# Kernel tuning notes

Measured on AMD Instinct MI355X. Metric: run time of the kernel, lower is better.

The kernel has to match this reference:

```python
import jax, jax.numpy as jnp
import numpy as np

B, T, C, H = 4, 4096, 1024, 64  # batch, seq, n_embd, head_size

def setup_inputs() -> dict:
    key = jax.random.key(0)
    kx, kq, kk, kv = jax.random.split(key, 4)
    x = jax.random.normal(kx, (B, T, C), dtype=jnp.float32)
    s = 1.0 / np.sqrt(C)
    Wq = jax.random.normal(kq, (C, H), dtype=jnp.float32) * s
    Wk = jax.random.normal(kk, (C, H), dtype=jnp.float32) * s
    Wv = jax.random.normal(kv, (C, H), dtype=jnp.float32) * s
    return {"x": x, "Wq": Wq, "Wk": Wk, "Wv": Wv}

def reference(x, Wq, Wk, Wv):
    B_, T_, C_ = x.shape
    q = x @ Wq  # [B,T,H]
    k = x @ Wk
    v = x @ Wv
    # NOTE: original scales by C**-0.5 (n_embd), not head_size**-0.5
    scale = jnp.asarray(C_, x.dtype) ** -0.5
    wei = jnp.einsum('bth,bsh->bts', q, k) * scale  # [B,T,T]
    causal = jnp.tril(jnp.ones((T_, T_), dtype=bool))
    wei = jnp.where(causal, wei, -jnp.inf)
    wei = jax.nn.softmax(wei, axis=-1)
    out = jnp.einsum('bts,bsh->bth', wei, v)  # [B,T,H]
    return out
```

## Files before the change

### kernel.cpp

```cpp
#include <hip/hip_runtime.h>
#include <hip/hip_bf16.h>
#include <math.h>

#define BB 4
#define TT 4096
#define CC 1024
#define HH 64

typedef __attribute__((ext_vector_type(8))) short short8;
typedef __attribute__((ext_vector_type(8))) unsigned short ushort8;
typedef __attribute__((ext_vector_type(4))) float f32x4;
typedef __attribute__((ext_vector_type(2))) unsigned int uint2v;
typedef __attribute__((ext_vector_type(4))) unsigned int uint4v;

__device__ inline unsigned short f2bf(float f) {
    unsigned int u = __builtin_bit_cast(unsigned int, f);
    unsigned int r = u + 0x7fffu + ((u >> 16) & 1u);
    return (unsigned short)(r >> 16);
}

__device__ inline unsigned int cvtpk(float lo, float hi) {
    unsigned int r;
    asm("v_cvt_pk_bf16_f32 %0, %1, %2" : "=v"(r) : "v"(lo), "v"(hi));
    return r;
}

__device__ inline int soff_strip(int qs) {
    if (qs < 128) return (qs - 64) * 2;
    if (qs < 192) return 128 + (qs - 128) * 3;
    return 320 + (qs - 192) * 4;
}

__global__ __launch_bounds__(256) void wtrans_kernel(
    const float* __restrict__ Wq,
    const float* __restrict__ Wk,
    const float* __restrict__ Wv,
    unsigned short* __restrict__ Wf)
{
    const int t = blockIdx.x * 256 + threadIdx.x;
    const int lane = t & 63;
    const int ntl  = (t >> 6) % 12;
    const int kt   = t / 768;
    const int quad = lane >> 4, n = lane & 15;
    const int m    = ntl >> 2;
    const int col  = (ntl & 3) * 16 + n;
    const float* src = (m == 0) ? Wq : (m == 1) ? Wk : Wv;
    ushort8 u;
#pragma unroll
    for (int j = 0; j < 8; ++j)
        u[j] = f2bf(src[(kt * 32 + quad * 8 + j) * 64 + col]);
    *(ushort8*)(Wf + (size_t)t * 8) = u;
}

__global__ __launch_bounds__(256, 4) void qkv_gemm(
    const float* __restrict__ x,
    const unsigned short* __restrict__ Wf,
    unsigned short* __restrict__ Qb,
    unsigned short* __restrict__ Kf,
    unsigned short* __restrict__ Vf)
{
    __shared__ __align__(16) unsigned char smem[25088];
    f32x4 (*red)[12][64] = (f32x4 (*)[12][64])smem;
    float (*Tl)[200]     = (float (*)[200])(smem + 12288);

    const int tid  = threadIdx.x;
    const int lane = tid & 63;
    const int wave = tid >> 6;
    const int n    = lane & 15;
    const int quad = lane >> 4;

    const int row0g = blockIdx.x * 16;
    const int b     = row0g >> 12;
    const int trow  = row0g & (TT - 1);
    const int st    = trow >> 6;
    const int mtb   = (trow >> 4) & 3;
    const int kkv   = (trow >> 5) & 1;
    const int vhalf = (trow >> 4) & 1;

    const float* xp0 = x + (size_t)(row0g + n) * CC + wave * 256 + quad * 8;

    f32x4 acc[12];
#pragma unroll
    for (int i = 0; i < 12; ++i) acc[i] = (f32x4){0.f, 0.f, 0.f, 0.f};

    float4 Pa[3][2];
#pragma unroll
    for (int s = 0; s < 3; ++s) {
        Pa[s][0] = *(const float4*)(xp0 + s * 32);
        Pa[s][1] = *(const float4*)(xp0 + s * 32 + 4);
    }

#pragma unroll
    for (int kt = 0; kt < 8; ++kt) {
        const int sl = kt % 3;

        uint4v u0;
        u0[0] = cvtpk(Pa[sl][0].x, Pa[sl][0].y);
        u0[1] = cvtpk(Pa[sl][0].z, Pa[sl][0].w);
        u0[2] = cvtpk(Pa[sl][1].x, Pa[sl][1].y);
        u0[3] = cvtpk(Pa[sl][1].z, Pa[sl][1].w);
        const short8 a0 = __builtin_bit_cast(short8, u0);

        if (kt + 3 < 8) {
            Pa[sl][0] = *(const float4*)(xp0 + (kt + 3) * 32);
            Pa[sl][1] = *(const float4*)(xp0 + (kt + 3) * 32 + 4);
        }

        const unsigned short* wp = Wf + ((size_t)((wave * 8 + kt) * 12) * 64 + lane) * 8;
#pragma unroll
        for (int ntl = 0; ntl < 12; ++ntl) {
            const short8 bw = *(const short8*)(wp + (size_t)ntl * 64 * 8);
            acc[ntl] = __builtin_amdgcn_mfma_f32_16x16x32_bf16(a0, bw, acc[ntl], 0, 0, 0);
        }
    }

    if (wave >= 2) {
#pragma unroll
        for (int ntl = 0; ntl < 12; ++ntl)
            red[wave - 2][ntl][lane] = acc[ntl];
    }
    __syncthreads();
    if (wave < 2) {
#pragma unroll
        for (int ntl = 0; ntl < 12; ++ntl)
            acc[ntl] += red[wave][ntl][lane];
    }
    __syncthreads();
    if (wave == 1) {
#pragma unroll
        for (int ntl = 0; ntl < 12; ++ntl)
            red[0][ntl][lane] = acc[ntl];
    }
    __syncthreads();
    if (wave == 0) {
#pragma unroll
        for (int ntl = 0; ntl < 12; ++ntl) {
            const f32x4 s = acc[ntl] + red[0][ntl][lane];
            const int col = (ntl >> 2) * 64 + (ntl & 3) * 16 + n;
#pragma unroll
            for (int r = 0; r < 4; ++r)
                Tl[quad * 4 + r][col] = s[r];
        }
    }
    __syncthreads();

    {
        const int row = tid & 15;
        const int c0  = (tid >> 4) * 4;
        unsigned int w0 = cvtpk(Tl[row][c0]     * 0.03125f, Tl[row][c0 + 1] * 0.03125f);
        unsigned int w1 = cvtpk(Tl[row][c0 + 2] * 0.03125f, Tl[row][c0 + 3] * 0.03125f);
        uint2v w; w[0] = w0; w[1] = w1;
        *(uint2v*)(Qb + (size_t)(row0g + row) * HH + c0) = w;
    }
    if (wave < 2) {
        const int kk = wave;
        ushort8 u;
#pragma unroll
        for (int j = 0; j < 8; ++j)
            u[j] = f2bf(Tl[n][64 + kk * 32 + quad * 8 + j]);
        const size_t r = (size_t)(((b * 64 + st) * 4 + mtb) * 2 + kk) * 64 + lane;
        *(ushort8*)(Kf + r * 8) = u;
    } else {
        const int hh = quad >> 1;
        const int ht = (wave - 2) * 2 + hh;
        const int qq = vhalf * 2 + (quad & 1);
        ushort8 u;
#pragma unroll
        for (int j = 0; j < 8; ++j)
            u[j] = f2bf(Tl[(quad & 1) * 8 + j][128 + ht * 16 + n]);
        const size_t r = (size_t)(((b * 64 + st) * 4 + ht) * 2 + kkv) * 64 + qq * 16 + n;
        *(ushort8*)(Vf + r * 8) = u;
    }
}

__global__ __launch_bounds__(256) void attn_kernel(
    const unsigned short* __restrict__ Qb,
    const unsigned short* __restrict__ Kf,
    const unsigned short* __restrict__ Vf,
    float* __restrict__ out,
    float* __restrict__ scr)
{
    __shared__ unsigned short Ps[4][2][16][72];

    const int tid  = threadIdx.x;
    const int lane = tid & 63;
    const int wave = tid >> 6;
    const int n    = lane & 15;
    const int quad = lane >> 4;

    const int wid = blockIdx.x * 4 + wave;
    const int b   = wid / 640;
    const int u   = wid - b * 640;

    int qs, ci;
    if (u < 64)        { qs = u;                  ci = 0; }
    else if (u < 192)  { const int v = u - 64;  qs = 64  + (v >> 1); ci = v & 1; }
    else if (u < 384)  { const int v = u - 192; const int d = v / 3;
                         qs = 128 + d;            ci = v - 3 * d; }
    else               { const int v = u - 384; qs = 192 + (v >> 2); ci = v & 3; }

    const int stmax = qs >> 2;
    const int st0   = ci << 4;
    const int stEnd = min(stmax, st0 + 15);
    const int nc    = (stmax + 16) >> 4;
    const int qrow  = qs * 16 + n;

    const unsigned short* qp = Qb + ((size_t)b * TT + qrow) * HH;
    const short8 bQ0 = *(const short8*)(qp + quad * 8);
    const short8 bQ1 = *(const short8*)(qp + 32 + quad * 8);

    const unsigned short* KfB = Kf + (size_t)b * 262144;
    const unsigned short* VfB = Vf + (size_t)b * 262144;

    f32x4 O[4];
#pragma unroll
    for (int ht = 0; ht < 4; ++ht) O[ht] = (f32x4){0.f, 0.f, 0.f, 0.f};
    float l = 0.f;

    short8 kA[4], kB[4];
#pragma unroll
    for (int mt = 0; mt < 4; ++mt) {
        const unsigned short* kp = KfB + (size_t)((st0 * 4 + mt) * 2) * 512 + lane * 8;
        kA[mt] = *(const short8*)(kp);
        kB[mt] = *(const short8*)(kp + 512);
    }

    for (int st = st0; st <= stEnd; ++st) {
        f32x4 S[4];
#pragma unroll
        for (int mt = 0; mt < 4; ++mt) {
            f32x4 acc = (f32x4){0.f, 0.f, 0.f, 0.f};
            acc = __builtin_amdgcn_mfma_f32_16x16x32_bf16(kA[mt], bQ0, acc, 0, 0, 0);
            acc = __builtin_amdgcn_mfma_f32_16x16x32_bf16(kB[mt], bQ1, acc, 0, 0, 0);
            S[mt] = acc;
        }

        short8 vA[4], vB[4];
#pragma unroll
        for (int ht = 0; ht < 4; ++ht) {
            const unsigned short* vp = VfB + (size_t)((st * 4 + ht) * 2) * 512 + lane * 8;
            vA[ht] = *(const short8*)(vp);
            vB[ht] = *(const short8*)(vp + 512);
        }
        if (st < stEnd) {
#pragma unroll
            for (int mt = 0; mt < 4; ++mt) {
                const unsigned short* kp = KfB + (size_t)(((st + 1) * 4 + mt) * 2) * 512 + lane * 8;
                kA[mt] = *(const short8*)(kp);
                kB[mt] = *(const short8*)(kp + 512);
            }
        }

        if (st == stmax) {
#pragma unroll
            for (int mt = 0; mt < 4; ++mt) {
                const int sg = st * 64 + mt * 16 + quad * 4;
#pragma unroll
                for (int r = 0; r < 4; ++r)
                    if (sg + r > qrow) S[mt][r] = -INFINITY;
            }
        }

#pragma unroll
        for (int mt = 0; mt < 4; ++mt)
#pragma unroll
            for (int r = 0; r < 4; ++r) {
                const float p = __expf(fminf(S[mt][r], 30.f));
                S[mt][r] = p;
                l += p;
            }

        const int pp = st & 1;
#pragma unroll
        for (int mt = 0; mt < 4; ++mt) {
            uint2v w;
            w[0] = (unsigned int)f2bf(S[mt][0]) | ((unsigned int)f2bf(S[mt][1]) << 16);
            w[1] = (unsigned int)f2bf(S[mt][2]) | ((unsigned int)f2bf(S[mt][3]) << 16);
            *(uint2v*)&Ps[wave][pp][n][mt * 16 + quad * 4] = w;
        }
        asm volatile("s_waitcnt lgkmcnt(0)" ::: "memory");
        const short8 bP0 = *(const short8*)&Ps[wave][pp][n][quad * 8];
        const short8 bP1 = *(const short8*)&Ps[wave][pp][n][32 + quad * 8];

#pragma unroll
        for (int ht = 0; ht < 4; ++ht) {
            O[ht] = __builtin_amdgcn_mfma_f32_16x16x32_bf16(vA[ht], bP0, O[ht], 0, 0, 0);
            O[ht] = __builtin_amdgcn_mfma_f32_16x16x32_bf16(vB[ht], bP1, O[ht], 0, 0, 0);
        }
    }

    l += __shfl_xor(l, 16);
    l += __shfl_xor(l, 32);

    if (nc == 1) {
        const float inv = 1.0f / l;
        float* op = out + ((size_t)b * TT + qrow) * HH;
#pragma unroll
        for (int ht = 0; ht < 4; ++ht) {
            float4 o4;
            o4.x = O[ht][0] * inv;
            o4.y = O[ht][1] * inv;
            o4.z = O[ht][2] * inv;
            o4.w = O[ht][3] * inv;
            *(float4*)(op + ht * 16 + quad * 4) = o4;
        }
    } else {
        float* sb = scr + (size_t)(b * 576 + soff_strip(qs) + ci) * 1040;
        float* rp = sb + n * 64;
#pragma unroll
        for (int ht = 0; ht < 4; ++ht)
            *(f32x4*)(rp + ht * 16 + quad * 4) = O[ht];
        if (quad == 0) sb[1024 + n] = l;
    }
}

__global__ __launch_bounds__(64) void combine_kernel(
    const float* __restrict__ scr,
    float* __restrict__ out)
{
    const int b  = blockIdx.x / 192;
    const int qs = 64 + blockIdx.x % 192;
    const int nc = ((qs >> 2) + 16) >> 4;
    const int base = b * 576 + soff_strip(qs);

    const int t    = threadIdx.x;
    const int row  = t >> 2;
    const int col0 = (t & 3) * 16;

    f32x4 s0 = (f32x4){0.f,0.f,0.f,0.f}, s1 = s0, s2 = s0, s3 = s0;
    float lsum = 0.f;
    for (int ci = 0; ci < nc; ++ci) {
        const float* sb = scr + (size_t)(base + ci) * 1040;
        lsum += sb[1024 + row];
        const float* p = sb + row * 64 + col0;
        s0 += *(const f32x4*)(p);
        s1 += *(const f32x4*)(p + 4);
        s2 += *(const f32x4*)(p + 8);
        s3 += *(const f32x4*)(p + 12);
    }
    const float inv = 1.0f / lsum;
    float* op = out + ((size_t)b * TT + qs * 16 + row) * HH + col0;
    *(f32x4*)(op)      = s0 * inv;
    *(f32x4*)(op + 4)  = s1 * inv;
    *(f32x4*)(op + 8)  = s2 * inv;
    *(f32x4*)(op + 12) = s3 * inv;
}

extern "C" void kernel_launch(void* const* d_in, const int* in_sizes, int n_in,
                              void* d_out, int out_size, void* d_ws, size_t ws_size,
                              hipStream_t stream)
{
    const float* x  = (const float*)d_in[0];
    const float* Wq = (const float*)d_in[1];
    const float* Wk = (const float*)d_in[2];
    const float* Wv = (const float*)d_in[3];

    unsigned short* Qb = (unsigned short*)d_ws;
    unsigned short* Wf = Qb + (size_t)BB * TT * HH;
    unsigned short* Kf = Wf + (size_t)192 * 1024;
    unsigned short* Vf = Kf + (size_t)BB * 262144;
    float*          scr = (float*)(Vf + (size_t)BB * 262144);
    float* out = (float*)d_out;

    wtrans_kernel<<<96, 256, 0, stream>>>(Wq, Wk, Wv, Wf);
    qkv_gemm<<<BB * TT / 16, 256, 0, stream>>>(x, Wf, Qb, Kf, Vf);
    attn_kernel<<<640, 256, 0, stream>>>(Qb, Kf, Vf, out, scr);
    combine_kernel<<<768, 64, 0, stream>>>(scr, out);
}
```

Before: 153.4 us.

## Restructure QKV GEMM into 64-row tiles with double-buffered LDS staging

The QKV projection kernel now handles 64 rows per block with 512 threads instead of 16 rows with 256. It stages x and weight tiles into LDS through asynchronous global_load_lds, double-buffered across 16 K-steps, and uses an XOR swizzle on the x tile. Each wave owns one 16-row m-tile and half of the 12 output n-tiles, so the cross-wave split-K reduction goes away. Each weight tile is now reused across four m-tiles rather than being reloaded from global memory per 16-row block. The cost is 80 KB of LDS per block, which limits occupancy, and 256 blocks may underfill the GPU.

```diff
diff --git a/kernel.cpp b/kernel.cpp
--- a/kernel.cpp
+++ b/kernel.cpp
@@ -23,6 +23,13 @@
     unsigned int r;
     asm("v_cvt_pk_bf16_f32 %0, %1, %2" : "=v"(r) : "v"(lo), "v"(hi));
     return r;
+}
+
+__device__ inline void gll16(const void* g, void* l) {
+    __builtin_amdgcn_global_load_lds(
+        (const __attribute__((address_space(1))) unsigned int*)g,
+        (__attribute__((address_space(3))) unsigned int*)l,
+        16, 0, 0);
 }
 
 __device__ inline int soff_strip(int qs) {
@@ -52,123 +59,123 @@
     *(ushort8*)(Wf + (size_t)t * 8) = u;
 }
 
-__global__ __launch_bounds__(256, 4) void qkv_gemm(
+__global__ __launch_bounds__(512, 2) void qkv_gemm(
     const float* __restrict__ x,
     const unsigned short* __restrict__ Wf,
     unsigned short* __restrict__ Qb,
     unsigned short* __restrict__ Kf,
     unsigned short* __restrict__ Vf)
 {
-    __shared__ __align__(16) unsigned char smem[25088];
-    f32x4 (*red)[12][64] = (f32x4 (*)[12][64])smem;
-    float (*Tl)[200]     = (float (*)[200])(smem + 12288);
+    __shared__ __align__(16) unsigned char smem[81920];
+    float (*Tl)[200] = (float (*)[200])smem;
 
     const int tid  = threadIdx.x;
     const int lane = tid & 63;
     const int wave = tid >> 6;
     const int n    = lane & 15;
     const int quad = lane >> 4;
-
-    const int row0g = blockIdx.x * 16;
+    const int mt   = wave & 3;
+    const int ch   = wave >> 2;
+
+    const int row0g = blockIdx.x * 64;
     const int b     = row0g >> 12;
-    const int trow  = row0g & (TT - 1);
-    const int st    = trow >> 6;
-    const int mtb   = (trow >> 4) & 3;
-    const int kkv   = (trow >> 5) & 1;
-    const int vhalf = (trow >> 4) & 1;
-
-    const float* xp0 = x + (size_t)(row0g + n) * CC + wave * 256 + quad * 8;
-
-    f32x4 acc[12];
-#pragma unroll
-    for (int i = 0; i < 12; ++i) acc[i] = (f32x4){0.f, 0.f, 0.f, 0.f};
-
-    float4 Pa[3][2];
-#pragma unroll
-    for (int s = 0; s < 3; ++s) {
-        Pa[s][0] = *(const float4*)(xp0 + s * 32);
-        Pa[s][1] = *(const float4*)(xp0 + s * 32 + 4);
-    }
-
-#pragma unroll
-    for (int kt = 0; kt < 8; ++kt) {
-        const int sl = kt % 3;
-
-        uint4v u0;
-        u0[0] = cvtpk(Pa[sl][0].x, Pa[sl][0].y);
-        u0[1] = cvtpk(Pa[sl][0].z, Pa[sl][0].w);
-        u0[2] = cvtpk(Pa[sl][1].x, Pa[sl][1].y);
-        u0[3] = cvtpk(Pa[sl][1].z, Pa[sl][1].w);
-        const short8 a0 = __builtin_bit_cast(short8, u0);
-
-        if (kt + 3 < 8) {
-            Pa[sl][0] = *(const float4*)(xp0 + (kt + 3) * 32);
-            Pa[sl][1] = *(const float4*)(xp0 + (kt + 3) * 32 + 4);
-        }
-
-        const unsigned short* wp = Wf + ((size_t)((wave * 8 + kt) * 12) * 64 + lane) * 8;
-#pragma unroll
-        for (int ntl = 0; ntl < 12; ++ntl) {
-            const short8 bw = *(const short8*)(wp + (size_t)ntl * 64 * 8);
-            acc[ntl] = __builtin_amdgcn_mfma_f32_16x16x32_bf16(a0, bw, acc[ntl], 0, 0, 0);
-        }
-    }
-
-    if (wave >= 2) {
-#pragma unroll
-        for (int ntl = 0; ntl < 12; ++ntl)
-            red[wave - 2][ntl][lane] = acc[ntl];
-    }
+    const int st    = (row0g & (TT - 1)) >> 6;
+
+    const char* xg = (const char*)(x + (size_t)row0g * CC);
+    const char* wg = (const char*)Wf;
+
+    f32x4 acc[6];
+#pragma unroll
+    for (int i = 0; i < 6; ++i) acc[i] = (f32x4){0.f, 0.f, 0.f, 0.f};
+
+    auto stage = [&](int bb, int s) {
+        unsigned char* base = smem + bb * 40960;
+#pragma unroll
+        for (int i = 0; i < 2; ++i) {
+            const int rr = (i * 8 + wave) * 4 + (lane >> 4);
+            const int cb = ((lane & 15) * 16) ^ ((rr & 7) << 4);
+            gll16(xg + (size_t)rr * 4096 + s * 256 + cb,
+                  base + (i * 8 + wave) * 1024);
+        }
+#pragma unroll
+        for (int i = 0; i < 3; ++i) {
+            const int off = (i * 8 + wave) * 1024;
+            gll16(wg + (size_t)s * 24576 + off + lane * 16,
+                  base + 16384 + off);
+        }
+    };
+
+    auto compute = [&](int bb) {
+        const unsigned char* xb = smem + bb * 40960;
+        const unsigned char* wb = xb + 16384;
+        const int row = mt * 16 + n;
+        const int swz = (n & 7) << 4;
+#pragma unroll
+        for (int ktl = 0; ktl < 2; ++ktl) {
+            const int c0 = (ktl * 128 + quad * 32) ^ swz;
+            const int c1 = (ktl * 128 + quad * 32 + 16) ^ swz;
+            const float4 f0 = *(const float4*)(xb + row * 256 + c0);
+            const float4 f1 = *(const float4*)(xb + row * 256 + c1);
+            uint4v u;
+            u[0] = cvtpk(f0.x, f0.y);
+            u[1] = cvtpk(f0.z, f0.w);
+            u[2] = cvtpk(f1.x, f1.y);
+            u[3] = cvtpk(f1.z, f1.w);
+            const short8 a0 = __builtin_bit_cast(short8, u);
+#pragma unroll
+            for (int t = 0; t < 6; ++t) {
+                const int g = ch * 6 + t;
+                const short8 bwv = *(const short8*)(wb + (ktl * 12 + g) * 1024 + lane * 16);
+                acc[t] = __builtin_amdgcn_mfma_f32_16x16x32_bf16(a0, bwv, acc[t], 0, 0, 0);
+            }
+        }
+    };
+
+    stage(0, 0);
     __syncthreads();
-    if (wave < 2) {
-#pragma unroll
-        for (int ntl = 0; ntl < 12; ++ntl)
-            acc[ntl] += red[wave][ntl][lane];
+#pragma unroll 2
+    for (int s = 0; s < 16; ++s) {
+        if (s + 1 < 16) stage((s + 1) & 1, s + 1);
+        compute(s & 1);
+        __syncthreads();
+    }
+
+#pragma unroll
+    for (int t = 0; t < 6; ++t) {
+        const int g   = ch * 6 + t;
+        const int col = (g >> 2) * 64 + (g & 3) * 16 + n;
+#pragma unroll
+        for (int r = 0; r < 4; ++r)
+            Tl[mt * 16 + quad * 4 + r][col] = acc[t][r];
     }
     __syncthreads();
-    if (wave == 1) {
-#pragma unroll
-        for (int ntl = 0; ntl < 12; ++ntl)
-            red[0][ntl][lane] = acc[ntl];
-    }
-    __syncthreads();
-    if (wave == 0) {
-#pragma unroll
-        for (int ntl = 0; ntl < 12; ++ntl) {
-            const f32x4 s = acc[ntl] + red[0][ntl][lane];
-            const int col = (ntl >> 2) * 64 + (ntl & 3) * 16 + n;
-#pragma unroll
-            for (int r = 0; r < 4; ++r)
-                Tl[quad * 4 + r][col] = s[r];
-        }
-    }
-    __syncthreads();
 
     {
-        const int row = tid & 15;
-        const int c0  = (tid >> 4) * 4;
-        unsigned int w0 = cvtpk(Tl[row][c0]     * 0.03125f, Tl[row][c0 + 1] * 0.03125f);
-        unsigned int w1 = cvtpk(Tl[row][c0 + 2] * 0.03125f, Tl[row][c0 + 3] * 0.03125f);
-        uint2v w; w[0] = w0; w[1] = w1;
-        *(uint2v*)(Qb + (size_t)(row0g + row) * HH + c0) = w;
-    }
-    if (wave < 2) {
-        const int kk = wave;
+        const int row = tid & 63;
+        const int c0  = (tid >> 6) * 8;
+        uint4v w4;
+        w4[0] = cvtpk(Tl[row][c0]     * 0.03125f, Tl[row][c0 + 1] * 0.03125f);
+        w4[1] = cvtpk(Tl[row][c0 + 2] * 0.03125f, Tl[row][c0 + 3] * 0.03125f);
+        w4[2] = cvtpk(Tl[row][c0 + 4] * 0.03125f, Tl[row][c0 + 5] * 0.03125f);
+        w4[3] = cvtpk(Tl[row][c0 + 6] * 0.03125f, Tl[row][c0 + 7] * 0.03125f);
+        *(uint4v*)(Qb + (size_t)(row0g + row) * HH + c0) = w4;
+    }
+    {
+        const int mt2 = wave >> 1, kk = wave & 1;
         ushort8 u;
 #pragma unroll
         for (int j = 0; j < 8; ++j)
-            u[j] = f2bf(Tl[n][64 + kk * 32 + quad * 8 + j]);
-        const size_t r = (size_t)(((b * 64 + st) * 4 + mtb) * 2 + kk) * 64 + lane;
+            u[j] = f2bf(Tl[mt2 * 16 + n][64 + kk * 32 + quad * 8 + j]);
+        const size_t r = (size_t)(((b * 64 + st) * 4 + mt2) * 2 + kk) * 64 + lane;
         *(ushort8*)(Kf + r * 8) = u;
-    } else {
-        const int hh = quad >> 1;
-        const int ht = (wave - 2) * 2 + hh;
-        const int qq = vhalf * 2 + (quad & 1);
+    }
+    {
+        const int ht = wave >> 1, kv = wave & 1;
         ushort8 u;
 #pragma unroll
         for (int j = 0; j < 8; ++j)
-            u[j] = f2bf(Tl[(quad & 1) * 8 + j][128 + ht * 16 + n]);
-        const size_t r = (size_t)(((b * 64 + st) * 4 + ht) * 2 + kkv) * 64 + qq * 16 + n;
+            u[j] = f2bf(Tl[kv * 32 + quad * 8 + j][128 + ht * 16 + n]);
+        const size_t r = (size_t)(((b * 64 + st) * 4 + ht) * 2 + kv) * 64 + lane;
         *(ushort8*)(Vf + r * 8) = u;
     }
 }
@@ -363,7 +370,7 @@
     float* out = (float*)d_out;
 
     wtrans_kernel<<<96, 256, 0, stream>>>(Wq, Wk, Wv, Wf);
-    qkv_gemm<<<BB * TT / 16, 256, 0, stream>>>(x, Wf, Qb, Kf, Vf);
+    qkv_gemm<<<BB * TT / 64, 512, 0, stream>>>(x, Wf, Qb, Kf, Vf);
     attn_kernel<<<640, 256, 0, stream>>>(Qb, Kf, Vf, out, scr);
     combine_kernel<<<768, 64, 0, stream>>>(scr, out);
 }
```

After: 150.0 us. -2.2%, faster.
